# Optimization experiments

Measured on AMD Instinct MI355X. Metric: run time of the kernel, lower is better.

Reference implementation:

```python
import jax, jax.numpy as jnp
import numpy as np

B, S, H, C = 512, 16, 501, 7


def _uniform(k, shape, scale):
    return jax.random.uniform(k, shape, minval=-scale, maxval=scale, dtype=jnp.float32)


def setup_inputs() -> dict:
    key = jax.random.key(0)
    ks = jax.random.split(key, 20)
    s = 1.0 / np.sqrt(H)        # torch default init bound for Linear(H, .) and GRUCell
    se = 1.0 / np.sqrt(2 * H)   # Linear(2H, 1)
    z = jax.random.normal(ks[0], (B, H), jnp.float32)
    # strictly-lower-triangular 0/1 adjacency (DAG, ancestors have smaller index)
    dep = jax.random.randint(ks[1], (B, S, S), 0, 2).astype(jnp.float32)
    dep_graph = dep * jnp.tril(jnp.ones((S, S), jnp.float32), k=-1)
    node_encoding = jax.nn.one_hot(jax.random.randint(ks[2], (B, S), 0, C), C, dtype=jnp.float32)
    return {
        "z": z,
        "dep_graph": dep_graph,
        "node_encoding": node_encoding,
        "W_lin1": _uniform(ks[3], (H, H), s), "b_lin1": _uniform(ks[4], (H,), s),
        "W_vert": _uniform(ks[5], (C, H), s), "b_vert": _uniform(ks[6], (C,), s),
        "W_edge": _uniform(ks[7], (1, 2 * H), se), "b_edge": _uniform(ks[8], (1,), se),
        "W_gate": _uniform(ks[9], (H, H), s), "b_gate": _uniform(ks[10], (H,), s),
        "W_map": _uniform(ks[11], (H, H), s), "b_map": _uniform(ks[12], (H,), s),
        "W_ih": _uniform(ks[13], (3 * H, C), s), "b_ih": _uniform(ks[14], (3 * H,), s),
        "W_hh": _uniform(ks[15], (3 * H, H), s), "b_hh": _uniform(ks[16], (3 * H,), s),
    }


def _forward(z, dep_graph, node_encoding, W_lin1, b_lin1, W_vert, b_vert, W_edge, b_edge,
             W_gate, b_gate, W_map, b_map, W_ih, b_ih, W_hh, b_hh):
    Bs, Ss, _ = dep_graph.shape
    Hs = W_lin1.shape[0]

    def gru(x, h):  # torch.nn.GRUCell math
        gi = x @ W_ih.T + b_ih
        gh = h @ W_hh.T + b_hh
        i_r, i_z, i_n = jnp.split(gi, 3, axis=-1)
        h_r, h_z, h_n = jnp.split(gh, 3, axis=-1)
        r = jax.nn.sigmoid(i_r + h_r)
        u = jax.nn.sigmoid(i_z + h_z)
        n = jnp.tanh(i_n + r * h_n)
        return (1.0 - u) * n + u * h

    col = jnp.arange(Ss)

    def outer_step(carry, idx):
        graph_state, nhs = carry  # nhs: (B, S, H) node_hidden_state
        logits = jax.nn.softmax(graph_state @ W_vert.T + b_vert, axis=-1)  # add_vertex
        x_idx = jax.lax.dynamic_index_in_dim(node_encoding, idx, axis=1, keepdims=False)  # (B, C)
        row0 = jax.lax.dynamic_index_in_dim(dep_graph, idx, axis=1, keepdims=False)       # (B, S)

        def inner_step(ic, t):  # v_j = idx-1, ..., 0 (masked when v_j < 0)
            hv, nhs_i, row, edges = ic
            v_j = idx - 1 - t
            active = v_j >= 0
            vj = jnp.maximum(v_j, 0)
            hidden_j = jax.lax.dynamic_index_in_dim(nhs_i, vj, axis=1, keepdims=False)  # (B, H)
            p = jax.nn.sigmoid(jnp.concatenate([hv, hidden_j], axis=-1) @ W_edge.T + b_edge)  # (B,1)
            is_edge = (p[:, 0] >= 0.5).astype(z.dtype)  # hard threshold, as in source
            # emulates the in-place `ancestors[:, :v_j] = 0` on the dep_graph row
            row_new = jnp.where(col[None, :] < vj, 0.0, row)
            anc = (nhs_i * row_new[:, :, None]).reshape(-1, Hs)  # (B*S, H)
            h_in = (jax.nn.sigmoid(anc @ W_gate.T + b_gate) * (anc @ W_map.T + b_map)
                    ).reshape(Bs, Ss, Hs).sum(axis=1)  # gated-sum message aggregation
            hv_new = gru(x_idx, h_in)
            nhs_new = jax.lax.dynamic_update_index_in_dim(nhs_i, hv_new, idx, axis=1)
            edges = jnp.where(active, edges.at[:, vj].set(is_edge), edges)
            hv = jnp.where(active, hv_new, hv)
            nhs_i = jnp.where(active, nhs_new, nhs_i)
            row = jnp.where(active, row_new, row)
            return (hv, nhs_i, row, edges), None

        edges0 = jnp.zeros((Bs, Ss), z.dtype)
        (hv, nhs2, _, edges), _ = jax.lax.scan(
            inner_step, (graph_state, nhs, row0, edges0), jnp.arange(Ss - 1))
        # index == 0: no ancestors; hv = GRU(x_0, graph_state) (source leaves hv undefined here)
        hv = jnp.where(idx == 0, gru(x_idx, graph_state), hv)
        nhs3 = jax.lax.dynamic_update_index_in_dim(nhs2, hv, idx, axis=1)
        return (hv, nhs3), (logits, edges)

    graph_state0 = z @ W_lin1.T + b_lin1
    nhs0 = jnp.zeros((Bs, Ss, Hs), z.dtype)
    _, (enc, rows) = jax.lax.scan(outer_step, (graph_state0, nhs0), jnp.arange(Ss))
    gen_dep_graph = jnp.transpose(rows, (1, 0, 2))      # (B, S, S)
    gen_node_encoding = jnp.transpose(enc, (1, 0, 2))   # (B, S, C)
    return gen_dep_graph, gen_node_encoding


def reference(z, dep_graph, node_encoding, W_lin1, b_lin1, W_vert, b_vert, W_edge, b_edge,
              W_gate, b_gate, W_map, b_map, W_ih, b_ih, W_hh, b_hh):
    return _forward(z, dep_graph, node_encoding, W_lin1, b_lin1, W_vert, b_vert, W_edge,
                    b_edge, W_gate, b_gate, W_map, b_map, W_ih, b_ih, W_hh, b_hh)
```

## Files before the change

kernel.cpp:

```cpp
#include <hip/hip_runtime.h>
#include <math.h>

#define BB 512
#define SS 16
#define HH 501
#define CC 7
#define KP 512
#define PBK (4*BB)
#define OFF_ENC (BB*SS*SS)

#define BUFSZ (132*PBK)
#define O_BUFIN 0
#define O_BUFH  BUFSZ
#define O_ALIST (2*BUFSZ)
#define O_ELIST (O_ALIST + SS*BB)
#define O_CLS   (O_ELIST + SS*BB)
#define O_ZT    (O_CLS + SS*BB)
#define O_INT   (O_ZT  + 262144)
#define O_HT    (O_INT + 262144)
#define O_WLIN  (O_HT  + 262144)
#define O_WPOST (O_WLIN + 262144)
#define O_WHH   (O_WPOST + 524288)
#define O_WDOT  (O_WHH + 786432)

typedef __attribute__((ext_vector_type(8))) short bfrag;
typedef __attribute__((ext_vector_type(4))) float ffrag;

__device__ __forceinline__ float sigm(float x) { return 1.f / (1.f + expf(-x)); }

__device__ __forceinline__ unsigned short f2bf(float x) {
    unsigned u = __float_as_uint(x);
    u = u + 0x7fffu + ((u >> 16) & 1u);
    return (unsigned short)(u >> 16);
}
__device__ __forceinline__ float bf2f(unsigned short h) {
    return __uint_as_float(((unsigned)h) << 16);
}

__global__ __launch_bounds__(256) void k_wprep(
    const float* __restrict__ Wlin1, const float* __restrict__ Wgate,
    const float* __restrict__ Wmap,  const float* __restrict__ Whh,
    const float* __restrict__ Wedge, const float* __restrict__ Wvert,
    unsigned short* __restrict__ wlin, unsigned short* __restrict__ wpost,
    unsigned short* __restrict__ whhf, unsigned short* __restrict__ wdot)
{
    const int id = blockIdx.x * 256 + threadIdx.x;
    const int slot = id >> 10, rem = id & 1023, s = rem >> 6, lane = rem & 63;
    const int rloc = lane & 15;
    const int k0 = s * 32 + ((lane >> 4) << 3);
    const float* src; unsigned short* dst; int dslot; bool valid;
    if (slot < 32) {
        int row = slot * 16 + rloc; valid = row < HH;
        src = Wlin1 + (size_t)(valid ? row : 0) * HH; dst = wlin; dslot = slot;
    } else if (slot < 96) {
        int p = slot - 32, g = p >> 5, mt = p & 31;
        int row = mt * 16 + rloc; valid = row < HH;
        src = (g ? Wmap : Wgate) + (size_t)(valid ? row : 0) * HH; dst = wpost; dslot = p;
    } else if (slot < 192) {
        int p = slot - 96, g = p >> 5, mt = p & 31;
        int row = mt * 16 + rloc; valid = row < HH;
        src = Whh + (size_t)(g * HH + (valid ? row : 0)) * HH; dst = whhf; dslot = p;
    } else {
        int row = rloc; dst = wdot; dslot = 0;
        if (row < 2)      { src = Wedge + (size_t)row * HH; valid = true; }
        else if (row < 9) { src = Wvert + (size_t)(row - 2) * HH; valid = true; }
        else              { src = Wedge; valid = false; }
    }
    unsigned h[8], l[8];
#pragma unroll
    for (int j = 0; j < 8; ++j) {
        int k = k0 + j;
        float w = (valid && k < HH) ? src[k] : 0.f;
        unsigned short hb = f2bf(w);
        h[j] = hb; l[j] = f2bf(w - bf2f(hb));
    }
    size_t base = ((size_t)dslot * 32 + s * 2) * 512 + lane * 8;
    uint4 uh, ul;
    uh.x = h[0] | (h[1] << 16); uh.y = h[2] | (h[3] << 16);
    uh.z = h[4] | (h[5] << 16); uh.w = h[6] | (h[7] << 16);
    ul.x = l[0] | (l[1] << 16); ul.y = l[2] | (l[3] << 16);
    ul.z = l[4] | (l[5] << 16); ul.w = l[6] | (l[7] << 16);
    *(uint4*)&dst[base] = uh;
    *(uint4*)&dst[base + 512] = ul;
}

__global__ __launch_bounds__(256) void k_prep2(
    const float* __restrict__ z, const float* __restrict__ xenc,
    unsigned short* __restrict__ zTh, unsigned short* __restrict__ zTl,
    int* __restrict__ cls, float* __restrict__ out)
{
    const int b = blockIdx.x, tid = threadIdx.x;
    if (b < 128) {
        const int id = b * 256 + tid;
        const int bb = id >> 6, kc = id & 63, k0 = kc * 8;
        unsigned h[8], l[8];
#pragma unroll
        for (int j = 0; j < 8; ++j) {
            int k = k0 + j;
            float w = (k < HH) ? z[(size_t)bb * HH + k] : 0.f;
            unsigned short hb = f2bf(w);
            h[j] = hb; l[j] = f2bf(w - bf2f(hb));
        }
        uint4 uh, ul;
        uh.x = h[0] | (h[1] << 16); uh.y = h[2] | (h[3] << 16);
        uh.z = h[4] | (h[5] << 16); uh.w = h[6] | (h[7] << 16);
        ul.x = l[0] | (l[1] << 16); ul.y = l[2] | (l[3] << 16);
        ul.z = l[4] | (l[5] << 16); ul.w = l[6] | (l[7] << 16);
        *(uint4*)&zTh[(size_t)bb * 512 + k0] = uh;
        *(uint4*)&zTl[(size_t)bb * 512 + k0] = ul;
    } else if (b < 136) {
        int base = (b - 128) * 1024 + tid * 4;
#pragma unroll
        for (int q = 0; q < 4; ++q) {
            int e = base + q, sI = e >> 9, bb = e & 511;
            const float* xp = xenc + ((size_t)bb * SS + sI) * CC;
            int cv = 0;
#pragma unroll
            for (int cc = 0; cc < CC; ++cc) if (xp[cc] > 0.5f) cv = cc;
            cls[sI * BB + bb] = cv;
        }
    } else {
        float4 z4 = make_float4(0.f, 0.f, 0.f, 0.f);
        float4* o4 = (float4*)out;
#pragma unroll
        for (int q = 0; q < 4; ++q)
            o4[(b - 136) * 1024 + q * 256 + tid] = z4;
    }
}

template<int G>
__device__ __forceinline__ void gemm_core(
    const unsigned short* __restrict__ wf,
    const unsigned short* __restrict__ bTh, const unsigned short* __restrict__ bTl,
    int mt0, int c0, int lane, ffrag* acc)
{
    const char* wp  = (const char*)wf  + (size_t)lane * 16;
    const char* bph = (const char*)bTh + (size_t)(c0 + (lane & 15)) * 1024 + ((lane >> 4) * 16);
    const char* bpl = (const char*)bTl + (size_t)(c0 + (lane & 15)) * 1024 + ((lane >> 4) * 16);
#pragma unroll
    for (int s = 0; s < 16; ++s) {
        bfrag bh[2], bl[2];
#pragma unroll
        for (int n = 0; n < 2; ++n) {
            bh[n] = *(const bfrag*)(bph + n * 16384 + s * 64);
            bl[n] = *(const bfrag*)(bpl + n * 16384 + s * 64);
        }
#pragma unroll
        for (int g = 0; g < G; ++g) {
#pragma unroll
            for (int m = 0; m < 2; ++m) {
                const char* ap = wp + (size_t)((g * 32 + mt0 + m) * 32 + s * 2) * 1024;
                bfrag ah = *(const bfrag*)ap;
                bfrag al = *(const bfrag*)(ap + 1024);
#pragma unroll
                for (int n = 0; n < 2; ++n) {
                    ffrag* A = acc + (g * 2 + m) * 2 + n;
                    *A = __builtin_amdgcn_mfma_f32_16x16x32_bf16(ah, bh[n], *A, 0, 0, 0);
                    *A = __builtin_amdgcn_mfma_f32_16x16x32_bf16(ah, bl[n], *A, 0, 0, 0);
                    *A = __builtin_amdgcn_mfma_f32_16x16x32_bf16(al, bh[n], *A, 0, 0, 0);
                }
            }
        }
    }
}

__device__ __forceinline__ void store_pack(float* __restrict__ dst, int rbase, int c, const float* v) {
    float* p = dst + (size_t)(rbase >> 2) * PBK + c * 4;
    if (rbase + 3 < HH) {
        *(float4*)p = make_float4(v[0], v[1], v[2], v[3]);
    } else {
#pragma unroll
        for (int i = 0; i < 4; ++i) if (rbase + i < HH) p[i] = v[i];
    }
}

__device__ __forceinline__ void store_T(unsigned short* __restrict__ Th, unsigned short* __restrict__ Tl,
                                        int c, int rbase, const float* v) {
    unsigned h[4], l[4];
#pragma unroll
    for (int i = 0; i < 4; ++i) {
        unsigned short hb = f2bf(v[i]);
        h[i] = hb; l[i] = f2bf(v[i] - bf2f(hb));
    }
    uint2 uh, ul;
    uh.x = h[0] | (h[1] << 16); uh.y = h[2] | (h[3] << 16);
    ul.x = l[0] | (l[1] << 16); ul.y = l[2] | (l[3] << 16);
    *(uint2*)&Th[(size_t)c * 512 + rbase] = uh;
    *(uint2*)&Tl[(size_t)c * 512 + rbase] = ul;
}

__global__ __launch_bounds__(128, 1) void k_g0m(
    const unsigned short* __restrict__ zTh, const unsigned short* __restrict__ zTl,
    const unsigned short* __restrict__ wlin, const float* __restrict__ blin1,
    float* __restrict__ dstPack, unsigned short* __restrict__ Th, unsigned short* __restrict__ Tl)
{
    const int tid = threadIdx.x, lane = tid & 63, wv = tid >> 6;
    const int rb = blockIdx.x >> 3, cbb = blockIdx.x & 7;
    const int mt0 = rb * 2, c0 = (cbb * 2 + wv) * 32;
    const ffrag fz = {0.f, 0.f, 0.f, 0.f};
    ffrag acc[4];
#pragma unroll
    for (int i = 0; i < 4; ++i) acc[i] = fz;
    gemm_core<1>(wlin, zTh, zTl, mt0, c0, lane, acc);
#pragma unroll
    for (int m = 0; m < 2; ++m) {
        const int rbase = (mt0 + m) * 16 + ((lane >> 4) << 2);
#pragma unroll
        for (int n = 0; n < 2; ++n) {
            const int c = c0 + n * 16 + (lane & 15);
            float v[4];
#pragma unroll
            for (int r = 0; r < 4; ++r) {
                int rr = rbase + r;
                v[r] = (rr < HH) ? acc[m * 2 + n][r] + blin1[rr] : 0.f;
            }
            store_pack(dstPack, rbase, c, v);
            store_T(Th, Tl, c, rbase, v);
        }
    }
}

__global__ __launch_bounds__(128, 1) void k_grum(
    const unsigned short* __restrict__ inTh, const unsigned short* __restrict__ inTl,
    const unsigned short* __restrict__ whhf, const float* __restrict__ hinPack,
    const int* __restrict__ cls, const float* __restrict__ Wih,
    const float* __restrict__ bih, const float* __restrict__ bhh,
    int idx, unsigned short* __restrict__ Th, unsigned short* __restrict__ Tl)
{
    const int tid = threadIdx.x, lane = tid & 63, wv = tid >> 6;
    const int rb = blockIdx.x >> 3, cbb = blockIdx.x & 7;
    const int mt0 = rb * 2, c0 = (cbb * 2 + wv) * 32;
    const ffrag fz = {0.f, 0.f, 0.f, 0.f};
    ffrag acc[12];
#pragma unroll
    for (int i = 0; i < 12; ++i) acc[i] = fz;
    gemm_core<3>(whhf, inTh, inTl, mt0, c0, lane, acc);
#pragma unroll
    for (int m = 0; m < 2; ++m) {
        const int rbase = (mt0 + m) * 16 + ((lane >> 4) << 2);
#pragma unroll
        for (int n = 0; n < 2; ++n) {
            const int c = c0 + n * 16 + (lane & 15);
            const int cc = cls[idx * BB + c];
            float hp[4];
            { float4 t = *(const float4*)&hinPack[(size_t)(rbase >> 2) * PBK + c * 4];
              hp[0] = t.x; hp[1] = t.y; hp[2] = t.z; hp[3] = t.w; }
            float v[4];
#pragma unroll
            for (int r = 0; r < 4; ++r) {
                int rr = rbase + r;
                if (rr < HH) {
                    float ar  = acc[(0 * 2 + m) * 2 + n][r];
                    float az  = acc[(1 * 2 + m) * 2 + n][r];
                    float an2 = acc[(2 * 2 + m) * 2 + n][r];
                    float rgt = sigm(Wih[(size_t)rr * CC + cc] + bih[rr] + ar + bhh[rr]);
                    float ugt = sigm(Wih[(size_t)(HH + rr) * CC + cc] + bih[HH + rr] + az + bhh[HH + rr]);
                    float ngt = tanhf(Wih[(size_t)(2 * HH + rr) * CC + cc] + bih[2 * HH + rr]
                                      + rgt * (an2 + bhh[2 * HH + rr]));
                    v[r] = (1.f - ugt) * ngt + ugt * hp[r];
                } else v[r] = 0.f;
            }
            store_T(Th, Tl, c, rbase, v);
        }
    }
}

__device__ __forceinline__ void dots_body(
    int blk8, int tid, int lane, int wv,
    const unsigned short* __restrict__ Th, const unsigned short* __restrict__ Tl,
    const unsigned short* __restrict__ wdot, const float* __restrict__ bvert,
    const float* __restrict__ bedge, float* __restrict__ Alist, float* __restrict__ Elist,
    int idx, float* __restrict__ out, float (*dls)[65])
{
    const int c0 = (blk8 * 2 + wv) * 32;
    const ffrag fz = {0.f, 0.f, 0.f, 0.f};
    ffrag acc[2]; acc[0] = fz; acc[1] = fz;
    const char* wp  = (const char*)wdot + (size_t)lane * 16;
    const char* bph = (const char*)Th + (size_t)(c0 + (lane & 15)) * 1024 + ((lane >> 4) * 16);
    const char* bpl = (const char*)Tl + (size_t)(c0 + (lane & 15)) * 1024 + ((lane >> 4) * 16);
#pragma unroll
    for (int s = 0; s < 16; ++s) {
        bfrag ah = *(const bfrag*)(wp + (size_t)(s * 2) * 1024);
        bfrag al = *(const bfrag*)(wp + (size_t)(s * 2 + 1) * 1024);
#pragma unroll
        for (int n = 0; n < 2; ++n) {
            bfrag bh = *(const bfrag*)(bph + n * 16384 + s * 64);
            bfrag bl = *(const bfrag*)(bpl + n * 16384 + s * 64);
            acc[n] = __builtin_amdgcn_mfma_f32_16x16x32_bf16(ah, bh, acc[n], 0, 0, 0);
            acc[n] = __builtin_amdgcn_mfma_f32_16x16x32_bf16(ah, bl, acc[n], 0, 0, 0);
            acc[n] = __builtin_amdgcn_mfma_f32_16x16x32_bf16(al, bh, acc[n], 0, 0, 0);
        }
    }
#pragma unroll
    for (int n = 0; n < 2; ++n)
#pragma unroll
        for (int r = 0; r < 4; ++r)
            dls[((lane >> 4) << 2) + r][wv * 32 + n * 16 + (lane & 15)] = acc[n][r];
    __syncthreads();
    if (tid < 64) {
        const int b = blk8 * 64 + tid;
        float v[9];
#pragma unroll
        for (int j = 0; j < 9; ++j) v[j] = dls[j][tid];
        if (idx >= 0) { Alist[idx * BB + b] = v[0]; Elist[idx * BB + b] = v[1]; }
        if (idx <= SS - 2) {
            float lv[CC], mx = -1e30f;
#pragma unroll
            for (int c = 0; c < CC; ++c) { lv[c] = v[2 + c] + bvert[c]; mx = fmaxf(mx, lv[c]); }
            float sum = 0.f, ev[CC];
#pragma unroll
            for (int c = 0; c < CC; ++c) { ev[c] = expf(lv[c] - mx); sum += ev[c]; }
            float inv = 1.f / sum;
#pragma unroll
            for (int c = 0; c < CC; ++c)
                out[OFF_ENC + ((size_t)b * SS + (idx + 1)) * CC + c] = ev[c] * inv;
        }
        if (idx >= 1) {
            float be = bedge[0];
            float aprev = Alist[(idx - 1) * BB + b], eprev = Elist[(idx - 1) * BB + b];
            out[(size_t)b * SS * SS + idx * SS + (idx - 1)] =
                (aprev + eprev + be >= 0.f) ? 1.f : 0.f;
            for (int vj = 0; vj <= idx - 2; ++vj)
                out[(size_t)b * SS * SS + idx * SS + vj] =
                    (v[0] + Elist[vj * BB + b] + be >= 0.f) ? 1.f : 0.f;
        }
    }
}

__global__ __launch_bounds__(128, 1) void k_dotsm(
    const unsigned short* __restrict__ Th, const unsigned short* __restrict__ Tl,
    const unsigned short* __restrict__ wdot, const float* __restrict__ bvert,
    const float* __restrict__ bedge, float* __restrict__ Alist, float* __restrict__ Elist,
    int idx, float* __restrict__ out)
{
    __shared__ float dls[16][65];
    dots_body(blockIdx.x, threadIdx.x, threadIdx.x & 63, threadIdx.x >> 6,
              Th, Tl, wdot, bvert, bedge, Alist, Elist, idx, out, dls);
}

__global__ __launch_bounds__(128, 1) void k_postm(
    const unsigned short* __restrict__ hTh, const unsigned short* __restrict__ hTl,
    const unsigned short* __restrict__ wpostf,
    const float* __restrict__ bgate, const float* __restrict__ bmap,
    const float* __restrict__ dep,
    const unsigned short* __restrict__ wdot, const float* __restrict__ bvert,
    const float* __restrict__ bedge, float* __restrict__ Alist, float* __restrict__ Elist,
    int idx, float* __restrict__ dstPack,
    unsigned short* __restrict__ Th, unsigned short* __restrict__ Tl,
    float* __restrict__ out)
{
    __shared__ float dls[16][65];
    const int tid = threadIdx.x, lane = tid & 63, wv = tid >> 6;
    if ((int)blockIdx.x < 128) {
        const int rb = blockIdx.x >> 3, cbb = blockIdx.x & 7;
        const int mt0 = rb * 2, c0 = (cbb * 2 + wv) * 32;
        const ffrag fz = {0.f, 0.f, 0.f, 0.f};
        ffrag acc[8];
#pragma unroll
        for (int i = 0; i < 8; ++i) acc[i] = fz;
        gemm_core<2>(wpostf, hTh, hTl, mt0, c0, lane, acc);
#pragma unroll
        for (int m = 0; m < 2; ++m) {
            const int rbase = (mt0 + m) * 16 + ((lane >> 4) << 2);
#pragma unroll
            for (int n = 0; n < 2; ++n) {
                const int c = c0 + n * 16 + (lane & 15);
                const float d = dep[(size_t)c * (SS * SS) + (idx + 1) * SS + idx];
                float v[4];
#pragma unroll
                for (int r = 0; r < 4; ++r) {
                    int rr = rbase + r;
                    if (rr < HH) {
                        float bg = bgate[rr], bm = bmap[rr];
                        float cv = sigm(bg) * bm;
                        float f = sigm(acc[(0 * 2 + m) * 2 + n][r] + bg)
                                * (acc[(1 * 2 + m) * 2 + n][r] + bm);
                        v[r] = (d != 0.f) ? (f + 15.f * cv) : (16.f * cv);
                    } else v[r] = 0.f;
                }
                store_pack(dstPack, rbase, c, v);
                store_T(Th, Tl, c, rbase, v);
            }
        }
    } else {
        dots_body((int)blockIdx.x - 128, tid, lane, wv,
                  hTh, hTl, wdot, bvert, bedge, Alist, Elist, idx, out, dls);
    }
}

extern "C" void kernel_launch(void* const* d_in, const int* in_sizes, int n_in,
                              void* d_out, int out_size, void* d_ws, size_t ws_size,
                              hipStream_t stream)
{
    const float* z     = (const float*)d_in[0];
    const float* dep   = (const float*)d_in[1];
    const float* xenc  = (const float*)d_in[2];
    const float* Wlin1 = (const float*)d_in[3];
    const float* blin1 = (const float*)d_in[4];
    const float* Wvert = (const float*)d_in[5];
    const float* bvert = (const float*)d_in[6];
    const float* Wedge = (const float*)d_in[7];
    const float* bedge = (const float*)d_in[8];
    const float* Wgate = (const float*)d_in[9];
    const float* bgate = (const float*)d_in[10];
    const float* Wmap  = (const float*)d_in[11];
    const float* bmap  = (const float*)d_in[12];
    const float* Wih   = (const float*)d_in[13];
    const float* bih   = (const float*)d_in[14];
    const float* Whh   = (const float*)d_in[15];
    const float* bhh   = (const float*)d_in[16];
    float* out = (float*)d_out;

    float* ws    = (float*)d_ws;
    float* bufIn = ws + O_BUFIN;
    float* Alist = ws + O_ALIST;
    float* Elist = ws + O_ELIST;
    int*   cls   = (int*)(ws + O_CLS);
    unsigned short* zTh  = (unsigned short*)(ws + O_ZT);
    unsigned short* zTl  = zTh + 262144;
    unsigned short* inTh = (unsigned short*)(ws + O_INT);
    unsigned short* inTl = inTh + 262144;
    unsigned short* hTh  = (unsigned short*)(ws + O_HT);
    unsigned short* hTl  = hTh + 262144;
    unsigned short* wlin  = (unsigned short*)(ws + O_WLIN);
    unsigned short* wpost = (unsigned short*)(ws + O_WPOST);
    unsigned short* whhf  = (unsigned short*)(ws + O_WHH);
    unsigned short* wdot  = (unsigned short*)(ws + O_WDOT);

    k_wprep<<<772, 256, 0, stream>>>(Wlin1, Wgate, Wmap, Whh, Wedge, Wvert,
                                     wlin, wpost, whhf, wdot);
    k_prep2<<<168, 256, 0, stream>>>(z, xenc, zTh, zTl, cls, out);
    k_g0m<<<128, 128, 0, stream>>>(zTh, zTl, wlin, blin1, bufIn, inTh, inTl);
    k_dotsm<<<8, 128, 0, stream>>>(inTh, inTl, wdot, bvert, bedge, Alist, Elist, -1, out);
    for (int idx = 0; idx < SS; ++idx) {
        k_grum<<<128, 128, 0, stream>>>(inTh, inTl, whhf, bufIn, cls, Wih, bih, bhh,
                                        idx, hTh, hTl);
        if (idx < SS - 1)
            k_postm<<<136, 128, 0, stream>>>(hTh, hTl, wpost, bgate, bmap, dep,
                                             wdot, bvert, bedge, Alist, Elist,
                                             idx, bufIn, inTh, inTl, out);
        else
            k_dotsm<<<8, 128, 0, stream>>>(hTh, hTl, wdot, bvert, bedge, Alist, Elist,
                                           idx, out);
    }
}
```

Measured before the change: 1.109 ms.

## Fuse all stages into one persistent kernel with grid barriers

Replaces the chain of about 35 separate launches (weight prep, z prep, initial linear, and a GRU/post/dots kernel pair per step) with a single persistent kernel of 264 blocks. The stages are separated by atomic grid-wide barriers. Each GEMM block now computes one 16-row tile instead of two, doubling the block count to 256 for better CU coverage. The initial dots pass overlaps with the first GRU step. This is meant to remove per-launch overhead and idle gaps between the many small dependent kernels. In exchange it adds spin-barrier latency, and correctness relies on all blocks being co-resident.

```diff
diff --git a/kernel.cpp b/kernel.cpp
--- a/kernel.cpp
+++ b/kernel.cpp
@@ -5,13 +5,11 @@
 #define SS 16
 #define HH 501
 #define CC 7
-#define KP 512
 #define PBK (4*BB)
 #define OFF_ENC (BB*SS*SS)
 
 #define BUFSZ (132*PBK)
 #define O_BUFIN 0
-#define O_BUFH  BUFSZ
 #define O_ALIST (2*BUFSZ)
 #define O_ELIST (O_ALIST + SS*BB)
 #define O_CLS   (O_ELIST + SS*BB)
@@ -22,6 +20,11 @@
 #define O_WPOST (O_WLIN + 262144)
 #define O_WHH   (O_WPOST + 524288)
 #define O_WDOT  (O_WHH + 786432)
+#define O_SYNC  (O_WDOT + 8192)
+
+#define NBLK 264
+#define NTHR 128
+#define NTOT (NBLK*NTHR)
 
 typedef __attribute__((ext_vector_type(8))) short bfrag;
 typedef __attribute__((ext_vector_type(4))) float ffrag;
@@ -37,14 +40,29 @@
     return __uint_as_float(((unsigned)h) << 16);
 }
 
-__global__ __launch_bounds__(256) void k_wprep(
+__device__ __forceinline__ void gridbar(int* __restrict__ bars, int id) {
+    __syncthreads();
+    if (threadIdx.x == 0) {
+        __threadfence();
+        __hip_atomic_fetch_add(&bars[id], 1, __ATOMIC_ACQ_REL, __HIP_MEMORY_SCOPE_AGENT);
+        while (__hip_atomic_load(&bars[id], __ATOMIC_ACQUIRE, __HIP_MEMORY_SCOPE_AGENT) < NBLK) {}
+        __threadfence();
+    }
+    __syncthreads();
+}
+
+__global__ void k_init(int* bars) {
+    bars[threadIdx.x] = 0;
+}
+
+__device__ __forceinline__ void wprep_item(
+    int id,
     const float* __restrict__ Wlin1, const float* __restrict__ Wgate,
     const float* __restrict__ Wmap,  const float* __restrict__ Whh,
     const float* __restrict__ Wedge, const float* __restrict__ Wvert,
     unsigned short* __restrict__ wlin, unsigned short* __restrict__ wpost,
     unsigned short* __restrict__ whhf, unsigned short* __restrict__ wdot)
 {
-    const int id = blockIdx.x * 256 + threadIdx.x;
     const int slot = id >> 10, rem = id & 1023, s = rem >> 6, lane = rem & 63;
     const int rloc = lane & 15;
     const int k0 = s * 32 + ((lane >> 4) << 3);
@@ -84,55 +102,33 @@
     *(uint4*)&dst[base + 512] = ul;
 }
 
-__global__ __launch_bounds__(256) void k_prep2(
-    const float* __restrict__ z, const float* __restrict__ xenc,
-    unsigned short* __restrict__ zTh, unsigned short* __restrict__ zTl,
-    int* __restrict__ cls, float* __restrict__ out)
-{
-    const int b = blockIdx.x, tid = threadIdx.x;
-    if (b < 128) {
-        const int id = b * 256 + tid;
-        const int bb = id >> 6, kc = id & 63, k0 = kc * 8;
-        unsigned h[8], l[8];
-#pragma unroll
-        for (int j = 0; j < 8; ++j) {
-            int k = k0 + j;
-            float w = (k < HH) ? z[(size_t)bb * HH + k] : 0.f;
-            unsigned short hb = f2bf(w);
-            h[j] = hb; l[j] = f2bf(w - bf2f(hb));
-        }
-        uint4 uh, ul;
-        uh.x = h[0] | (h[1] << 16); uh.y = h[2] | (h[3] << 16);
-        uh.z = h[4] | (h[5] << 16); uh.w = h[6] | (h[7] << 16);
-        ul.x = l[0] | (l[1] << 16); ul.y = l[2] | (l[3] << 16);
-        ul.z = l[4] | (l[5] << 16); ul.w = l[6] | (l[7] << 16);
-        *(uint4*)&zTh[(size_t)bb * 512 + k0] = uh;
-        *(uint4*)&zTl[(size_t)bb * 512 + k0] = ul;
-    } else if (b < 136) {
-        int base = (b - 128) * 1024 + tid * 4;
-#pragma unroll
-        for (int q = 0; q < 4; ++q) {
-            int e = base + q, sI = e >> 9, bb = e & 511;
-            const float* xp = xenc + ((size_t)bb * SS + sI) * CC;
-            int cv = 0;
-#pragma unroll
-            for (int cc = 0; cc < CC; ++cc) if (xp[cc] > 0.5f) cv = cc;
-            cls[sI * BB + bb] = cv;
-        }
-    } else {
-        float4 z4 = make_float4(0.f, 0.f, 0.f, 0.f);
-        float4* o4 = (float4*)out;
-#pragma unroll
-        for (int q = 0; q < 4; ++q)
-            o4[(b - 136) * 1024 + q * 256 + tid] = z4;
-    }
+__device__ __forceinline__ void prepz_item(
+    int id, const float* __restrict__ z,
+    unsigned short* __restrict__ zTh, unsigned short* __restrict__ zTl)
+{
+    const int bb = id >> 6, kc = id & 63, k0 = kc * 8;
+    unsigned h[8], l[8];
+#pragma unroll
+    for (int j = 0; j < 8; ++j) {
+        int k = k0 + j;
+        float w = (k < HH) ? z[(size_t)bb * HH + k] : 0.f;
+        unsigned short hb = f2bf(w);
+        h[j] = hb; l[j] = f2bf(w - bf2f(hb));
+    }
+    uint4 uh, ul;
+    uh.x = h[0] | (h[1] << 16); uh.y = h[2] | (h[3] << 16);
+    uh.z = h[4] | (h[5] << 16); uh.w = h[6] | (h[7] << 16);
+    ul.x = l[0] | (l[1] << 16); ul.y = l[2] | (l[3] << 16);
+    ul.z = l[4] | (l[5] << 16); ul.w = l[6] | (l[7] << 16);
+    *(uint4*)&zTh[(size_t)bb * 512 + k0] = uh;
+    *(uint4*)&zTl[(size_t)bb * 512 + k0] = ul;
 }
 
 template<int G>
-__device__ __forceinline__ void gemm_core(
+__device__ __forceinline__ void gemm_core1(
     const unsigned short* __restrict__ wf,
     const unsigned short* __restrict__ bTh, const unsigned short* __restrict__ bTl,
-    int mt0, int c0, int lane, ffrag* acc)
+    int mt, int c0, int lane, ffrag* acc)
 {
     const char* wp  = (const char*)wf  + (size_t)lane * 16;
     const char* bph = (const char*)bTh + (size_t)(c0 + (lane & 15)) * 1024 + ((lane >> 4) * 16);
@@ -147,18 +143,15 @@
         }
 #pragma unroll
         for (int g = 0; g < G; ++g) {
-#pragma unroll
-            for (int m = 0; m < 2; ++m) {
-                const char* ap = wp + (size_t)((g * 32 + mt0 + m) * 32 + s * 2) * 1024;
-                bfrag ah = *(const bfrag*)ap;
-                bfrag al = *(const bfrag*)(ap + 1024);
-#pragma unroll
-                for (int n = 0; n < 2; ++n) {
-                    ffrag* A = acc + (g * 2 + m) * 2 + n;
-                    *A = __builtin_amdgcn_mfma_f32_16x16x32_bf16(ah, bh[n], *A, 0, 0, 0);
-                    *A = __builtin_amdgcn_mfma_f32_16x16x32_bf16(ah, bl[n], *A, 0, 0, 0);
-                    *A = __builtin_amdgcn_mfma_f32_16x16x32_bf16(al, bh[n], *A, 0, 0, 0);
-                }
+            const char* ap = wp + (size_t)((g * 32 + mt) * 32 + s * 2) * 1024;
+            bfrag ah = *(const bfrag*)ap;
+            bfrag al = *(const bfrag*)(ap + 1024);
+#pragma unroll
+            for (int n = 0; n < 2; ++n) {
+                ffrag* A = acc + g * 2 + n;
+                *A = __builtin_amdgcn_mfma_f32_16x16x32_bf16(ah, bh[n], *A, 0, 0, 0);
+                *A = __builtin_amdgcn_mfma_f32_16x16x32_bf16(ah, bl[n], *A, 0, 0, 0);
+                *A = __builtin_amdgcn_mfma_f32_16x16x32_bf16(al, bh[n], *A, 0, 0, 0);
             }
         }
     }
@@ -189,79 +182,105 @@
     *(uint2*)&Tl[(size_t)c * 512 + rbase] = ul;
 }
 
-__global__ __launch_bounds__(128, 1) void k_g0m(
+__device__ __forceinline__ void g0_body(
+    int bid, int lane, int wv,
     const unsigned short* __restrict__ zTh, const unsigned short* __restrict__ zTl,
     const unsigned short* __restrict__ wlin, const float* __restrict__ blin1,
     float* __restrict__ dstPack, unsigned short* __restrict__ Th, unsigned short* __restrict__ Tl)
 {
-    const int tid = threadIdx.x, lane = tid & 63, wv = tid >> 6;
-    const int rb = blockIdx.x >> 3, cbb = blockIdx.x & 7;
-    const int mt0 = rb * 2, c0 = (cbb * 2 + wv) * 32;
+    const int mt = bid >> 3, c0 = ((bid & 7) * 2 + wv) * 32;
     const ffrag fz = {0.f, 0.f, 0.f, 0.f};
-    ffrag acc[4];
-#pragma unroll
-    for (int i = 0; i < 4; ++i) acc[i] = fz;
-    gemm_core<1>(wlin, zTh, zTl, mt0, c0, lane, acc);
-#pragma unroll
-    for (int m = 0; m < 2; ++m) {
-        const int rbase = (mt0 + m) * 16 + ((lane >> 4) << 2);
-#pragma unroll
-        for (int n = 0; n < 2; ++n) {
-            const int c = c0 + n * 16 + (lane & 15);
-            float v[4];
-#pragma unroll
-            for (int r = 0; r < 4; ++r) {
-                int rr = rbase + r;
-                v[r] = (rr < HH) ? acc[m * 2 + n][r] + blin1[rr] : 0.f;
-            }
-            store_pack(dstPack, rbase, c, v);
-            store_T(Th, Tl, c, rbase, v);
-        }
-    }
-}
-
-__global__ __launch_bounds__(128, 1) void k_grum(
+    ffrag acc[2]; acc[0] = fz; acc[1] = fz;
+    gemm_core1<1>(wlin, zTh, zTl, mt, c0, lane, acc);
+    const int rbase = mt * 16 + ((lane >> 4) << 2);
+#pragma unroll
+    for (int n = 0; n < 2; ++n) {
+        const int c = c0 + n * 16 + (lane & 15);
+        float v[4];
+#pragma unroll
+        for (int r = 0; r < 4; ++r) {
+            int rr = rbase + r;
+            v[r] = (rr < HH) ? acc[n][r] + blin1[rr] : 0.f;
+        }
+        store_pack(dstPack, rbase, c, v);
+        store_T(Th, Tl, c, rbase, v);
+    }
+}
+
+__device__ __forceinline__ void gru_body(
+    int bid, int lane, int wv,
     const unsigned short* __restrict__ inTh, const unsigned short* __restrict__ inTl,
     const unsigned short* __restrict__ whhf, const float* __restrict__ hinPack,
     const int* __restrict__ cls, const float* __restrict__ Wih,
     const float* __restrict__ bih, const float* __restrict__ bhh,
     int idx, unsigned short* __restrict__ Th, unsigned short* __restrict__ Tl)
 {
-    const int tid = threadIdx.x, lane = tid & 63, wv = tid >> 6;
-    const int rb = blockIdx.x >> 3, cbb = blockIdx.x & 7;
-    const int mt0 = rb * 2, c0 = (cbb * 2 + wv) * 32;
+    const int mt = bid >> 3, c0 = ((bid & 7) * 2 + wv) * 32;
     const ffrag fz = {0.f, 0.f, 0.f, 0.f};
-    ffrag acc[12];
-#pragma unroll
-    for (int i = 0; i < 12; ++i) acc[i] = fz;
-    gemm_core<3>(whhf, inTh, inTl, mt0, c0, lane, acc);
-#pragma unroll
-    for (int m = 0; m < 2; ++m) {
-        const int rbase = (mt0 + m) * 16 + ((lane >> 4) << 2);
-#pragma unroll
-        for (int n = 0; n < 2; ++n) {
-            const int c = c0 + n * 16 + (lane & 15);
-            const int cc = cls[idx * BB + c];
-            float hp[4];
-            { float4 t = *(const float4*)&hinPack[(size_t)(rbase >> 2) * PBK + c * 4];
-              hp[0] = t.x; hp[1] = t.y; hp[2] = t.z; hp[3] = t.w; }
-            float v[4];
-#pragma unroll
-            for (int r = 0; r < 4; ++r) {
-                int rr = rbase + r;
-                if (rr < HH) {
-                    float ar  = acc[(0 * 2 + m) * 2 + n][r];
-                    float az  = acc[(1 * 2 + m) * 2 + n][r];
-                    float an2 = acc[(2 * 2 + m) * 2 + n][r];
-                    float rgt = sigm(Wih[(size_t)rr * CC + cc] + bih[rr] + ar + bhh[rr]);
-                    float ugt = sigm(Wih[(size_t)(HH + rr) * CC + cc] + bih[HH + rr] + az + bhh[HH + rr]);
-                    float ngt = tanhf(Wih[(size_t)(2 * HH + rr) * CC + cc] + bih[2 * HH + rr]
-                                      + rgt * (an2 + bhh[2 * HH + rr]));
-                    v[r] = (1.f - ugt) * ngt + ugt * hp[r];
-                } else v[r] = 0.f;
-            }
-            store_T(Th, Tl, c, rbase, v);
-        }
+    ffrag acc[6];
+#pragma unroll
+    for (int i = 0; i < 6; ++i) acc[i] = fz;
+    gemm_core1<3>(whhf, inTh, inTl, mt, c0, lane, acc);
+    const int rbase = mt * 16 + ((lane >> 4) << 2);
+#pragma unroll
+    for (int n = 0; n < 2; ++n) {
+        const int c = c0 + n * 16 + (lane & 15);
+        const int cc = cls[idx * BB + c];
+        float hp[4];
+        { float4 t = *(const float4*)&hinPack[(size_t)(rbase >> 2) * PBK + c * 4];
+          hp[0] = t.x; hp[1] = t.y; hp[2] = t.z; hp[3] = t.w; }
+        float v[4];
+#pragma unroll
+        for (int r = 0; r < 4; ++r) {
+            int rr = rbase + r;
+            if (rr < HH) {
+                float ar  = acc[0 * 2 + n][r];
+                float az  = acc[1 * 2 + n][r];
+                float an2 = acc[2 * 2 + n][r];
+                float rgt = sigm(Wih[(size_t)rr * CC + cc] + bih[rr] + ar + bhh[rr]);
+                float ugt = sigm(Wih[(size_t)(HH + rr) * CC + cc] + bih[HH + rr] + az + bhh[HH + rr]);
+                float ngt = tanhf(Wih[(size_t)(2 * HH + rr) * CC + cc] + bih[2 * HH + rr]
+                                  + rgt * (an2 + bhh[2 * HH + rr]));
+                v[r] = (1.f - ugt) * ngt + ugt * hp[r];
+            } else v[r] = 0.f;
+        }
+        store_T(Th, Tl, c, rbase, v);
+    }
+}
+
+__device__ __forceinline__ void post_body(
+    int bid, int lane, int wv,
+    const unsigned short* __restrict__ hTh, const unsigned short* __restrict__ hTl,
+    const unsigned short* __restrict__ wpostf,
+    const float* __restrict__ bgate, const float* __restrict__ bmap,
+    const float* __restrict__ dep, int idx,
+    float* __restrict__ dstPack,
+    unsigned short* __restrict__ Th, unsigned short* __restrict__ Tl)
+{
+    const int mt = bid >> 3, c0 = ((bid & 7) * 2 + wv) * 32;
+    const ffrag fz = {0.f, 0.f, 0.f, 0.f};
+    ffrag acc[4];
+#pragma unroll
+    for (int i = 0; i < 4; ++i) acc[i] = fz;
+    gemm_core1<2>(wpostf, hTh, hTl, mt, c0, lane, acc);
+    const int rbase = mt * 16 + ((lane >> 4) << 2);
+#pragma unroll
+    for (int n = 0; n < 2; ++n) {
+        const int c = c0 + n * 16 + (lane & 15);
+        const float d = dep[(size_t)c * (SS * SS) + (idx + 1) * SS + idx];
+        float v[4];
+#pragma unroll
+        for (int r = 0; r < 4; ++r) {
+            int rr = rbase + r;
+            if (rr < HH) {
+                float bg = bgate[rr], bm = bmap[rr];
+                float cv = sigm(bg) * bm;
+                float f = sigm(acc[0 * 2 + n][r] + bg) * (acc[1 * 2 + n][r] + bm);
+                v[r] = (d != 0.f) ? (f + 15.f * cv) : (16.f * cv);
+            } else v[r] = 0.f;
+        }
+        store_pack(dstPack, rbase, c, v);
+        store_T(Th, Tl, c, rbase, v);
     }
 }
 
@@ -325,66 +344,83 @@
                     (v[0] + Elist[vj * BB + b] + be >= 0.f) ? 1.f : 0.f;
         }
     }
-}
-
-__global__ __launch_bounds__(128, 1) void k_dotsm(
-    const unsigned short* __restrict__ Th, const unsigned short* __restrict__ Tl,
-    const unsigned short* __restrict__ wdot, const float* __restrict__ bvert,
-    const float* __restrict__ bedge, float* __restrict__ Alist, float* __restrict__ Elist,
-    int idx, float* __restrict__ out)
+    __syncthreads();
+}
+
+__global__ __launch_bounds__(NTHR, 1) void k_fused(
+    const float* z, const float* dep, const float* xenc,
+    const float* Wlin1, const float* blin1,
+    const float* Wvert, const float* bvert,
+    const float* Wedge, const float* bedge,
+    const float* Wgate, const float* bgate,
+    const float* Wmap,  const float* bmap,
+    const float* Wih,   const float* bih,
+    const float* Whh,   const float* bhh,
+    float* out, float* ws)
 {
     __shared__ float dls[16][65];
-    dots_body(blockIdx.x, threadIdx.x, threadIdx.x & 63, threadIdx.x >> 6,
-              Th, Tl, wdot, bvert, bedge, Alist, Elist, idx, out, dls);
-}
-
-__global__ __launch_bounds__(128, 1) void k_postm(
-    const unsigned short* __restrict__ hTh, const unsigned short* __restrict__ hTl,
-    const unsigned short* __restrict__ wpostf,
-    const float* __restrict__ bgate, const float* __restrict__ bmap,
-    const float* __restrict__ dep,
-    const unsigned short* __restrict__ wdot, const float* __restrict__ bvert,
-    const float* __restrict__ bedge, float* __restrict__ Alist, float* __restrict__ Elist,
-    int idx, float* __restrict__ dstPack,
-    unsigned short* __restrict__ Th, unsigned short* __restrict__ Tl,
-    float* __restrict__ out)
-{
-    __shared__ float dls[16][65];
-    const int tid = threadIdx.x, lane = tid & 63, wv = tid >> 6;
-    if ((int)blockIdx.x < 128) {
-        const int rb = blockIdx.x >> 3, cbb = blockIdx.x & 7;
-        const int mt0 = rb * 2, c0 = (cbb * 2 + wv) * 32;
-        const ffrag fz = {0.f, 0.f, 0.f, 0.f};
-        ffrag acc[8];
-#pragma unroll
-        for (int i = 0; i < 8; ++i) acc[i] = fz;
-        gemm_core<2>(wpostf, hTh, hTl, mt0, c0, lane, acc);
-#pragma unroll
-        for (int m = 0; m < 2; ++m) {
-            const int rbase = (mt0 + m) * 16 + ((lane >> 4) << 2);
-#pragma unroll
-            for (int n = 0; n < 2; ++n) {
-                const int c = c0 + n * 16 + (lane & 15);
-                const float d = dep[(size_t)c * (SS * SS) + (idx + 1) * SS + idx];
-                float v[4];
-#pragma unroll
-                for (int r = 0; r < 4; ++r) {
-                    int rr = rbase + r;
-                    if (rr < HH) {
-                        float bg = bgate[rr], bm = bmap[rr];
-                        float cv = sigm(bg) * bm;
-                        float f = sigm(acc[(0 * 2 + m) * 2 + n][r] + bg)
-                                * (acc[(1 * 2 + m) * 2 + n][r] + bm);
-                        v[r] = (d != 0.f) ? (f + 15.f * cv) : (16.f * cv);
-                    } else v[r] = 0.f;
-                }
-                store_pack(dstPack, rbase, c, v);
-                store_T(Th, Tl, c, rbase, v);
-            }
-        }
-    } else {
-        dots_body((int)blockIdx.x - 128, tid, lane, wv,
-                  hTh, hTl, wdot, bvert, bedge, Alist, Elist, idx, out, dls);
+
+    float* bufIn = ws + O_BUFIN;
+    float* Alist = ws + O_ALIST;
+    float* Elist = ws + O_ELIST;
+    int*   cls   = (int*)(ws + O_CLS);
+    unsigned short* zTh  = (unsigned short*)(ws + O_ZT);
+    unsigned short* zTl  = zTh + 262144;
+    unsigned short* inTh = (unsigned short*)(ws + O_INT);
+    unsigned short* inTl = inTh + 262144;
+    unsigned short* hTh  = (unsigned short*)(ws + O_HT);
+    unsigned short* hTl  = hTh + 262144;
+    unsigned short* wlin  = (unsigned short*)(ws + O_WLIN);
+    unsigned short* wpost = (unsigned short*)(ws + O_WPOST);
+    unsigned short* whhf  = (unsigned short*)(ws + O_WHH);
+    unsigned short* wdot  = (unsigned short*)(ws + O_WDOT);
+    int* bars = (int*)(ws + O_SYNC);
+
+    const int bid = blockIdx.x, tid = threadIdx.x;
+    const int lane = tid & 63, wv = tid >> 6;
+    const int gt = bid * NTHR + tid;
+    int barid = 0;
+
+    for (int i = gt; i < 193 * 1024; i += NTOT)
+        wprep_item(i, Wlin1, Wgate, Wmap, Whh, Wedge, Wvert, wlin, wpost, whhf, wdot);
+    for (int i = gt; i < 32768; i += NTOT)
+        prepz_item(i, z, zTh, zTl);
+    for (int i = gt; i < 8192; i += NTOT) {
+        int sI = i >> 9, bb = i & 511;
+        const float* xp = xenc + ((size_t)bb * SS + sI) * CC;
+        int cv = 0;
+#pragma unroll
+        for (int cc = 0; cc < CC; ++cc) if (xp[cc] > 0.5f) cv = cc;
+        cls[sI * BB + bb] = cv;
+    }
+    {
+        float4 z4 = make_float4(0.f, 0.f, 0.f, 0.f);
+        float4* o4 = (float4*)out;
+        for (int i = gt; i < 32768; i += NTOT) o4[i] = z4;
+    }
+    gridbar(bars, barid++);
+
+    if (bid < 256)
+        g0_body(bid, lane, wv, zTh, zTl, wlin, blin1, bufIn, inTh, inTl);
+    gridbar(bars, barid++);
+
+    for (int idx = 0; idx < SS; ++idx) {
+        if (bid < 256)
+            gru_body(bid, lane, wv, inTh, inTl, whhf, bufIn, cls, Wih, bih, bhh,
+                     idx, hTh, hTl);
+        else if (idx == 0)
+            dots_body(bid - 256, tid, lane, wv, inTh, inTl, wdot, bvert, bedge,
+                      Alist, Elist, -1, out, dls);
+        gridbar(bars, barid++);
+        if (bid < 256) {
+            if (idx < SS - 1)
+                post_body(bid, lane, wv, hTh, hTl, wpost, bgate, bmap, dep, idx,
+                          bufIn, inTh, inTl);
+        } else {
+            dots_body(bid - 256, tid, lane, wv, hTh, hTl, wdot, bvert, bedge,
+                      Alist, Elist, idx, out, dls);
+        }
+        if (idx < SS - 1) gridbar(bars, barid++);
     }
 }
 
@@ -410,37 +446,11 @@
     const float* Whh   = (const float*)d_in[15];
     const float* bhh   = (const float*)d_in[16];
     float* out = (float*)d_out;
-
-    float* ws    = (float*)d_ws;
-    float* bufIn = ws + O_BUFIN;
-    float* Alist = ws + O_ALIST;
-    float* Elist = ws + O_ELIST;
-    int*   cls   = (int*)(ws + O_CLS);
-    unsigned short* zTh  = (unsigned short*)(ws + O_ZT);
-    unsigned short* zTl  = zTh + 262144;
-    unsigned short* inTh = (unsigned short*)(ws + O_INT);
-    unsigned short* inTl = inTh + 262144;
-    unsigned short* hTh  = (unsigned short*)(ws + O_HT);
-    unsigned short* hTl  = hTh + 262144;
-    unsigned short* wlin  = (unsigned short*)(ws + O_WLIN);
-    unsigned short* wpost = (unsigned short*)(ws + O_WPOST);
-    unsigned short* whhf  = (unsigned short*)(ws + O_WHH);
-    unsigned short* wdot  = (unsigned short*)(ws + O_WDOT);
-
-    k_wprep<<<772, 256, 0, stream>>>(Wlin1, Wgate, Wmap, Whh, Wedge, Wvert,
-                                     wlin, wpost, whhf, wdot);
-    k_prep2<<<168, 256, 0, stream>>>(z, xenc, zTh, zTl, cls, out);
-    k_g0m<<<128, 128, 0, stream>>>(zTh, zTl, wlin, blin1, bufIn, inTh, inTl);
-    k_dotsm<<<8, 128, 0, stream>>>(inTh, inTl, wdot, bvert, bedge, Alist, Elist, -1, out);
-    for (int idx = 0; idx < SS; ++idx) {
-        k_grum<<<128, 128, 0, stream>>>(inTh, inTl, whhf, bufIn, cls, Wih, bih, bhh,
-                                        idx, hTh, hTl);
-        if (idx < SS - 1)
-            k_postm<<<136, 128, 0, stream>>>(hTh, hTl, wpost, bgate, bmap, dep,
-                                             wdot, bvert, bedge, Alist, Elist,
-                                             idx, bufIn, inTh, inTl, out);
-        else
-            k_dotsm<<<8, 128, 0, stream>>>(hTh, hTl, wdot, bvert, bedge, Alist, Elist,
-                                           idx, out);
-    }
-}
+    float* ws  = (float*)d_ws;
+
+    int* bars = (int*)(ws + O_SYNC);
+    k_init<<<1, 64, 0, stream>>>(bars);
+    k_fused<<<NBLK, NTHR, 0, stream>>>(z, dep, xenc, Wlin1, blin1, Wvert, bvert,
+                                       Wedge, bedge, Wgate, bgate, Wmap, bmap,
+                                       Wih, bih, Whh, bhh, out, ws);
+}
```

New measurement: 2.830 ms. +155.1%, slower.
